# Performance work log

Measured on AMD Instinct MI355X. Metric: run time of the kernel, lower is better.

Reference implementation:

```python
import jax, jax.numpy as jnp
import numpy as np

L, B, T, TC, T1, D, DK, FF = 4, 4, 1024, 1024, 2048, 384, 256, 1536
TT = 0.1   # lamed blending coefficient (tt in (0,1] path)
EPS = 1e-5


def _ln(x, g, b):
    m = jnp.mean(x, axis=-1, keepdims=True)
    v = jnp.mean((x - m) ** 2, axis=-1, keepdims=True)
    return (x - m) * jax.lax.rsqrt(v + EPS) * g + b


def setup_inputs() -> dict:
    key = jax.random.key(0)
    ks = jax.random.split(key, 16)
    s = 0.02
    return {
        "tgt": jax.random.normal(ks[0], (B, T, D), jnp.float32),
        "memory": jax.random.normal(ks[1], (B, T1, DK), jnp.float32),
        "score_c": jax.random.normal(ks[2], (L, B, TC, T1), jnp.float32),
        "out_c": jax.random.normal(ks[3], (L, B, TC, D), jnp.float32),
        "Wq": jax.random.normal(ks[4], (L, D, D), jnp.float32) * s,
        "bq": jnp.zeros((L, D), jnp.float32),
        "Wk": jax.random.normal(ks[5], (L, D, DK), jnp.float32) * s,
        "bk": jnp.zeros((L, D), jnp.float32),
        "Wv": jax.random.normal(ks[6], (L, D, DK), jnp.float32) * s,
        "bv": jnp.zeros((L, D), jnp.float32),
        "Wkn": jax.random.normal(ks[7], (L, D, D), jnp.float32) * s,
        "bkn": jnp.zeros((L, D), jnp.float32),
        "Wun": jax.random.normal(ks[8], (L, D, D), jnp.float32) * s,
        "bun": jnp.zeros((L, D), jnp.float32),
        "W1": jax.random.normal(ks[9], (L, FF, D), jnp.float32) * s,
        "b1": jnp.zeros((L, FF), jnp.float32),
        "W2": jax.random.normal(ks[10], (L, D, FF), jnp.float32) * s,
        "b2": jnp.zeros((L, D), jnp.float32),
        "g1": jnp.ones((L, D), jnp.float32),
        "be1": jnp.zeros((L, D), jnp.float32),
        "g2": jnp.ones((L, D), jnp.float32),
        "be2": jnp.zeros((L, D), jnp.float32),
    }


def reference(tgt, memory, score_c, out_c, Wq, bq, Wk, bk, Wv, bv,
              Wkn, bkn, Wun, bun, W1, b1, W2, b2, g1, be1, g2, be2):
    scale = 1.0 / np.sqrt(D)
    x = tgt
    for l in range(L):  # fixed small layer count
        # cross-attention q/k/v (n_head = 1)
        q = jnp.einsum('btd,ed->bte', x, Wq[l]) + bq[l]            # [B,T,D]
        k = jnp.einsum('bsk,ek->bse', memory, Wk[l]) + bk[l]       # [B,T1,D]
        v = jnp.einsum('bsk,ek->bse', memory, Wv[l]) + bv[l]       # [B,T1,D]
        att = jnp.einsum('bte,bse->bts', q, k) * scale             # [B,T,T1]
        # blended score path (tt in (0,1])
        unk = jnp.einsum('btd,ed->bte', x, Wun[l]) + bun[l]        # [B,T,D]
        kno = jnp.einsum('bcd,ed->bce', out_c[l], Wkn[l]) + bkn[l] # [B,TC,D]
        score1 = jnp.einsum('bte,bce->btc', unk, kno) * scale      # [B,T,TC]
        mixed = jnp.einsum('btc,bcs->bts', score1, score_c[l])     # [B,T,T1]
        blended = TT * jax.nn.softmax(mixed, axis=-1) \
                  + (1.0 - TT) * jax.nn.softmax(att, axis=-1)
        z = jnp.einsum('bts,bse->bte', blended, v)                 # [B,T,D]
        x = _ln(x + z, g1[l], be1[l])
        h = jax.nn.relu(jnp.einsum('btd,fd->btf', x, W1[l]) + b1[l])
        y2 = jnp.einsum('btf,df->btd', h, W2[l]) + b2[l]
        x = _ln(x + y2, g2[l], be2[l])
    return x
```

## Files before the change

### kernel.cpp

```cpp
#include <hip/hip_runtime.h>
#include <math.h>

#define Lc 4
#define Bc 4
#define Tc 1024
#define TCc 1024
#define T1c 2048
#define Dc 384
#define DKc 256
#define FFc 1536
#define TTc 0.1f
#define EPSc 1e-5f

typedef unsigned short u16;
typedef __attribute__((ext_vector_type(8))) __bf16 bf16x8;
typedef __attribute__((ext_vector_type(4))) float f32x4;

__device__ inline u16 f2bf(float f) {
  union { float f; unsigned u; } x; x.f = f;
  unsigned r = x.u + 0x7fffu + ((x.u >> 16) & 1u);
  return (u16)(r >> 16);
}

struct CDesc { const float* src; u16* dst; long n4; };
struct CPack { CDesc d[16]; long tot4; int nd; };

__global__ void cvt_multi(CPack P) {
  long i = (long)blockIdx.x * 256 + threadIdx.x;
  const long st = (long)gridDim.x * 256;
  for (; i < P.tot4; i += st) {
    long r = i; int g = 0;
    while (g < P.nd - 1 && r >= P.d[g].n4) { r -= P.d[g].n4; ++g; }
    float4 v = ((const float4*)P.d[g].src)[r];
    ushort4 o;
    o.x = f2bf(v.x); o.y = f2bf(v.y); o.z = f2bf(v.z); o.w = f2bf(v.w);
    ((ushort4*)P.d[g].dst)[r] = o;
  }
}

__global__ void concat_bias(const float* __restrict__ a, const float* __restrict__ b,
                            float* __restrict__ o) {
  int l = blockIdx.x, t = threadIdx.x;
  o[l * 768 + t] = (t < Dc) ? a[l * Dc + t] : b[l * Dc + t - Dc];
}

__global__ __launch_bounds__(256) void transpose_cvt(const float* __restrict__ src,
                                                     u16* __restrict__ dst) {
  __shared__ float t[64 * 65];
  const int z = blockIdx.z;
  const float* s = src + (long)z * TCc * T1c;
  u16* d = dst + (long)z * T1c * TCc;
  const int s0 = blockIdx.x * 64, c0 = blockIdx.y * 64;
  const int tc = threadIdx.x >> 4;
  const int tx = (threadIdx.x & 15) * 4;
#pragma unroll
  for (int it = 0; it < 4; ++it) {
    const int c = tc + it * 16;
    float4 v = *(const float4*)(s + (long)(c0 + c) * T1c + s0 + tx);
    float* q = t + c * 65 + tx;
    q[0] = v.x; q[1] = v.y; q[2] = v.z; q[3] = v.w;
  }
  __syncthreads();
#pragma unroll
  for (int it = 0; it < 4; ++it) {
    const int srow = tc + it * 16;
    u16 o[4];
#pragma unroll
    for (int k2 = 0; k2 < 4; ++k2) o[k2] = f2bf(t[(tx + k2) * 65 + srow]);
    *(ushort4*)(d + (long)(s0 + srow) * TCc + c0 + tx) = *(ushort4*)o;
  }
}

template<int BIAS_MODE, int RELU, int OUT_MODE, int SWIZ>
__global__ __launch_bounds__(256) void gemm_bt(
    const u16* __restrict__ A, const u16* __restrict__ B,
    void* __restrict__ C, const float* __restrict__ bias,
    float alpha, int N, int K, int lda, int ldb,
    long sA, long sB, long sC, long sBias, int ksplit, long sSlab)
{
  __shared__ __attribute__((aligned(16))) u16 As[128 * 32];
  __shared__ __attribute__((aligned(16))) u16 Bs[128 * 32];
  const int bz = blockIdx.z;
  const int b = bz / ksplit;
  const int kc = bz - b * ksplit;
  const int Klen = K / ksplit;
  const int k0 = kc * Klen;
  const u16* Ab = A + (long)b * sA;
  const u16* Bb = B + (long)b * sB;
  long tm, tn;
  if (SWIZ) {
    const int id = blockIdx.y * 16 + blockIdx.x;
    tm = (long)(id >> 4) * 128;
    tn = (long)(2 * (id & 7) + ((id >> 3) & 1)) * 128;
  } else {
    tm = (long)blockIdx.y * 128; tn = (long)blockIdx.x * 128;
  }
  const int tid = threadIdx.x;
  const int lane = tid & 63, wv = tid >> 6;
  const int wm = (wv >> 1) * 64, wn = (wv & 1) * 64;
  const int q = lane >> 4, r = lane & 15;
  const int ldr = lane >> 2;
  const int ldc = (lane & 3) * 8;

  const u16* gA0 = Ab + (tm + wv * 32 + ldr) * (long)lda + k0 + ldc;
  const u16* gA1 = gA0 + 16 * (long)lda;
  const u16* gB0 = Bb + (tn + wv * 32 + ldr) * (long)ldb + k0 + ldc;
  const u16* gB1 = gB0 + 16 * (long)ldb;
  u16* dA0 = As + (wv * 32 + ldr) * 32 + ldc;
  u16* dA1 = dA0 + 16 * 32;
  u16* dB0 = Bs + (wv * 32 + ldr) * 32 + ldc;
  u16* dB1 = dB0 + 16 * 32;

  const f32x4 zero4 = {0.0f, 0.0f, 0.0f, 0.0f};
  f32x4 acc[4][4];
#pragma unroll
  for (int i = 0; i < 4; ++i)
#pragma unroll
    for (int j = 0; j < 4; ++j) acc[i][j] = zero4;

  uint4 ra0 = *(const uint4*)gA0;
  uint4 ra1 = *(const uint4*)gA1;
  uint4 rb0 = *(const uint4*)gB0;
  uint4 rb1 = *(const uint4*)gB1;

  const int iters = Klen >> 5;
  for (int it = 0; it < iters; ++it) {
    __builtin_amdgcn_s_barrier();
    *(uint4*)dA0 = ra0; *(uint4*)dA1 = ra1;
    *(uint4*)dB0 = rb0; *(uint4*)dB1 = rb1;
    __syncthreads();
    if (it + 1 < iters) {
      const long o = (long)(it + 1) * 32;
      ra0 = *(const uint4*)(gA0 + o);
      ra1 = *(const uint4*)(gA1 + o);
      rb0 = *(const uint4*)(gB0 + o);
      rb1 = *(const uint4*)(gB1 + o);
    }
    bf16x8 af[4], bfr[4];
#pragma unroll
    for (int i = 0; i < 4; ++i) {
      af[i]  = *(const bf16x8*)(As + (wm + i * 16 + r) * 32 + q * 8);
      bfr[i] = *(const bf16x8*)(Bs + (wn + i * 16 + r) * 32 + q * 8);
    }
#pragma unroll
    for (int i = 0; i < 4; ++i)
#pragma unroll
      for (int j = 0; j < 4; ++j)
        acc[i][j] = __builtin_amdgcn_mfma_f32_16x16x32_bf16(af[i], bfr[j], acc[i][j], 0, 0, 0);
  }

  const float* biasb = bias ? bias + (long)b * sBias : nullptr;
#pragma unroll
  for (int i = 0; i < 4; ++i)
#pragma unroll
    for (int j = 0; j < 4; ++j)
#pragma unroll
      for (int v = 0; v < 4; ++v) {
        long row = tm + wm + i * 16 + q * 4 + v;
        long col = tn + wn + j * 16 + r;
        float val = acc[i][j][v] * alpha;
        if (BIAS_MODE == 1 && kc == 0) val += biasb[col];
        if (BIAS_MODE == 2 && kc == 0) val += biasb[row];
        if (RELU) val = fmaxf(val, 0.0f);
        long idx = (long)kc * sSlab + (long)b * sC + row * (long)N + col;
        if (OUT_MODE == 0)      ((float*)C)[idx] = val;
        else if (OUT_MODE == 1) ((u16*)C)[idx] = f2bf(val);
        else                    ((_Float16*)C)[idx] = (_Float16)val;
      }
}

__global__ __launch_bounds__(256) void blend_softmax(
    const _Float16* __restrict__ att, const _Float16* __restrict__ mixed,
    u16* __restrict__ out)
{
  const long row = blockIdx.x;
  const int tid = threadIdx.x;
  const _Float16* ar = att + row * T1c;
  const _Float16* mr = mixed + row * T1c;
  float a[8], m[8];
#pragma unroll
  for (int i = 0; i < 8; ++i) {
    a[i] = (float)ar[tid + i * 256];
    m[i] = (float)mr[tid + i * 256];
  }
  float amax = a[0], mmax = m[0];
#pragma unroll
  for (int i = 1; i < 8; ++i) { amax = fmaxf(amax, a[i]); mmax = fmaxf(mmax, m[i]); }
#pragma unroll
  for (int off = 32; off > 0; off >>= 1) {
    amax = fmaxf(amax, __shfl_xor(amax, off));
    mmax = fmaxf(mmax, __shfl_xor(mmax, off));
  }
  __shared__ float red[8];
  const int lane = tid & 63, wv = tid >> 6;
  if (lane == 0) { red[wv] = amax; red[4 + wv] = mmax; }
  __syncthreads();
  amax = fmaxf(fmaxf(red[0], red[1]), fmaxf(red[2], red[3]));
  mmax = fmaxf(fmaxf(red[4], red[5]), fmaxf(red[6], red[7]));
  __syncthreads();
  float asum = 0.f, msum = 0.f;
#pragma unroll
  for (int i = 0; i < 8; ++i) {
    a[i] = __expf(a[i] - amax); asum += a[i];
    m[i] = __expf(m[i] - mmax); msum += m[i];
  }
#pragma unroll
  for (int off = 32; off > 0; off >>= 1) {
    asum += __shfl_xor(asum, off);
    msum += __shfl_xor(msum, off);
  }
  if (lane == 0) { red[wv] = asum; red[4 + wv] = msum; }
  __syncthreads();
  asum = red[0] + red[1] + red[2] + red[3];
  msum = red[4] + red[5] + red[6] + red[7];
  const float ca = (1.0f - TTc) / asum, cm = TTc / msum;
#pragma unroll
  for (int i = 0; i < 8; ++i)
    out[row * T1c + tid + i * 256] = f2bf(a[i] * ca + m[i] * cm);
}

__global__ __launch_bounds__(384) void add_ln4(
    const float* __restrict__ xin, const float* __restrict__ zs,
    const float* __restrict__ g, const float* __restrict__ be,
    float* __restrict__ xout, u16* __restrict__ xbf)
{
  const long row = blockIdx.x;
  const int d = threadIdx.x;
  const long SL = (long)Bc * Tc * Dc;
  const long o = row * Dc + d;
  float v = xin[o] + zs[o] + zs[SL + o] + zs[2 * SL + o] + zs[3 * SL + o];
  float s = v, s2 = v * v;
#pragma unroll
  for (int off = 32; off > 0; off >>= 1) {
    s  += __shfl_xor(s, off);
    s2 += __shfl_xor(s2, off);
  }
  __shared__ float red[12];
  const int lane = d & 63, wv = d >> 6;
  if (lane == 0) { red[wv] = s; red[6 + wv] = s2; }
  __syncthreads();
  float S = 0.f, S2 = 0.f;
#pragma unroll
  for (int w = 0; w < 6; ++w) { S += red[w]; S2 += red[6 + w]; }
  const float mean = S * (1.0f / Dc);
  const float var  = S2 * (1.0f / Dc) - mean * mean;
  const float rstd = rsqrtf(var + EPSc);
  const float y = (v - mean) * rstd * g[d] + be[d];
  xout[o] = y;
  xbf[o] = f2bf(y);
}

extern "C" void kernel_launch(void* const* d_in, const int* in_sizes, int n_in,
                              void* d_out, int out_size, void* d_ws, size_t ws_size,
                              hipStream_t stream)
{
  const float* tgt     = (const float*)d_in[0];
  const float* memory  = (const float*)d_in[1];
  const float* score_c = (const float*)d_in[2];
  const float* out_c   = (const float*)d_in[3];
  const float* Wq  = (const float*)d_in[4];  const float* bq  = (const float*)d_in[5];
  const float* Wk  = (const float*)d_in[6];  const float* bk  = (const float*)d_in[7];
  const float* Wv  = (const float*)d_in[8];  const float* bv  = (const float*)d_in[9];
  const float* Wkn = (const float*)d_in[10]; const float* bkn = (const float*)d_in[11];
  const float* Wun = (const float*)d_in[12]; const float* bun = (const float*)d_in[13];
  const float* W1  = (const float*)d_in[14]; const float* b1  = (const float*)d_in[15];
  const float* W2  = (const float*)d_in[16]; const float* b2  = (const float*)d_in[17];
  const float* g1  = (const float*)d_in[18]; const float* be1 = (const float*)d_in[19];
  const float* g2  = (const float*)d_in[20]; const float* be2 = (const float*)d_in[21];
  (void)in_sizes; (void)n_in; (void)out_size;

  char* p = (char*)d_ws;
  auto alloc = [&](size_t b) { char* r = p; p += (b + 255) & ~(size_t)255; return r; };

  u16* wk_bf   = (u16*)alloc((size_t)Lc * Dc * DKc * 2);
  u16* wv_bf   = (u16*)alloc((size_t)Lc * Dc * DKc * 2);
  u16* wkn_bf  = (u16*)alloc((size_t)Lc * Dc * Dc * 2);
  u16* w1_bf   = (u16*)alloc((size_t)Lc * FFc * Dc * 2);
  u16* w2_bf   = (u16*)alloc((size_t)Lc * Dc * FFc * 2);
  u16* wqu_bf  = (u16*)alloc((size_t)Lc * 2 * Dc * Dc * 2);
  float* bqu   = (float*)alloc((size_t)Lc * 2 * Dc * 4);
  u16* mem_bf  = (u16*)alloc((size_t)Bc * T1c * DKc * 2);
  u16* outc_bf = (u16*)alloc((size_t)Lc * Bc * TCc * Dc * 2);
  u16* x_bf    = (u16*)alloc((size_t)Bc * Tc * Dc * 2);
  float* xbuf  = (float*)alloc((size_t)Bc * Tc * Dc * 4);
  u16* qunk_bf = (u16*)alloc((size_t)Bc * Tc * 2 * Dc * 2);
  u16* k_all   = (u16*)alloc((size_t)Bc * T1c * Lc * Dc * 2);
  u16* vT_all  = (u16*)alloc((size_t)Bc * Lc * Dc * T1c * 2);
  u16* kno_all = (u16*)alloc((size_t)Lc * Bc * TCc * Dc * 2);
  u16* s1_bf   = (u16*)alloc((size_t)Bc * Tc * TCc * 2);
  u16* scT_all = (u16*)alloc((size_t)Lc * Bc * T1c * TCc * 2);
  _Float16* att   = (_Float16*)alloc((size_t)Bc * Tc * T1c * 2);
  _Float16* mixed = (_Float16*)alloc((size_t)Bc * Tc * T1c * 2);
  u16* blended = (u16*)alloc((size_t)Bc * Tc * T1c * 2);
  float* zslab = (float*)alloc((size_t)4 * Bc * Tc * Dc * 4);
  float* yslab = (float*)alloc((size_t)4 * Bc * Tc * Dc * 4);
  u16* h_bf    = (u16*)alloc((size_t)Bc * Tc * FFc * 2);

  if ((size_t)(p - (char*)d_ws) > ws_size) return;

  {
    CPack cp{}; int g = 0; long tot4 = 0;
    auto add = [&](const float* s, u16* d, long n) {
      cp.d[g].src = s; cp.d[g].dst = d; cp.d[g].n4 = n / 4; tot4 += n / 4; ++g;
    };
    add(Wk,  wk_bf,  (long)Lc * Dc * DKc);
    add(Wv,  wv_bf,  (long)Lc * Dc * DKc);
    add(Wkn, wkn_bf, (long)Lc * Dc * Dc);
    add(W1,  w1_bf,  (long)Lc * FFc * Dc);
    add(W2,  w2_bf,  (long)Lc * Dc * FFc);
    add(memory, mem_bf, (long)Bc * T1c * DKc);
    add(out_c, outc_bf, (long)Lc * Bc * TCc * Dc);
    add(tgt, x_bf, (long)Bc * Tc * Dc);
    for (int l = 0; l < Lc; ++l) {
      add(Wq + (long)l * Dc * Dc,  wqu_bf + (long)l * 2 * Dc * Dc, (long)Dc * Dc);
      add(Wun + (long)l * Dc * Dc, wqu_bf + (long)l * 2 * Dc * Dc + Dc * Dc, (long)Dc * Dc);
    }
    cp.nd = g; cp.tot4 = tot4;
    cvt_multi<<<4096, 256, 0, stream>>>(cp);
  }
  concat_bias<<<Lc, 2 * Dc, 0, stream>>>(bq, bun, bqu);

  transpose_cvt<<<dim3(T1c / 64, TCc / 64, Lc * Bc), 256, 0, stream>>>(score_c, scT_all);

  const float scale = 1.0f / sqrtf((float)Dc);
  const long SLAB = (long)Bc * Tc * Dc;

  gemm_bt<1,0,1,0><<<dim3(Lc*Dc/128, Bc*T1c/128, 1), 256, 0, stream>>>(
      mem_bf, wk_bf, k_all, bk, 1.0f, Lc*Dc, DKc, DKc, DKc, 0, 0, 0, 0, 1, 0);
  gemm_bt<2,0,1,0><<<dim3(T1c/128, Lc*Dc/128, Bc), 256, 0, stream>>>(
      wv_bf, mem_bf, vT_all, bv, 1.0f, T1c, DKc, DKc, DKc,
      0, (long)T1c*DKc, (long)Lc*Dc*T1c, 0, 1, 0);
  gemm_bt<1,0,1,0><<<dim3(Dc/128, Bc*TCc/128, Lc), 256, 0, stream>>>(
      outc_bf, wkn_bf, kno_all, bkn, 1.0f, Dc, Dc, Dc, Dc,
      (long)Bc*TCc*Dc, (long)Dc*Dc, (long)Bc*TCc*Dc, Dc, 1, 0);

  for (int l = 0; l < Lc; ++l) {
    gemm_bt<1,0,1,0><<<dim3(2*Dc/128, Bc*Tc/128, 1), 256, 0, stream>>>(
        x_bf, wqu_bf + (long)l*2*Dc*Dc, qunk_bf, bqu + l*2*Dc,
        1.0f, 2*Dc, Dc, Dc, Dc, 0, 0, 0, 0, 1, 0);
    gemm_bt<0,0,2,0><<<dim3(T1c/128, Tc/128, Bc), 256, 0, stream>>>(
        qunk_bf, k_all + l*Dc, att, nullptr, scale, T1c, Dc, 2*Dc, Lc*Dc,
        (long)Tc*2*Dc, (long)T1c*Lc*Dc, (long)Tc*T1c, 0, 1, 0);
    gemm_bt<0,0,1,0><<<dim3(TCc/128, Tc/128, Bc), 256, 0, stream>>>(
        qunk_bf + Dc, kno_all + (long)l*Bc*TCc*Dc, s1_bf, nullptr, scale,
        TCc, Dc, 2*Dc, Dc, (long)Tc*2*Dc, (long)TCc*Dc, (long)Tc*TCc, 0, 1, 0);
    gemm_bt<0,0,2,1><<<dim3(T1c/128, Tc/128, Bc), 256, 0, stream>>>(
        s1_bf, scT_all + (long)l*Bc*T1c*TCc, mixed, nullptr, 1.0f,
        T1c, TCc, TCc, TCc, (long)Tc*TCc, (long)T1c*TCc, (long)Tc*T1c, 0, 1, 0);
    blend_softmax<<<Bc*Tc, 256, 0, stream>>>(att, mixed, blended);
    gemm_bt<0,0,0,0><<<dim3(Dc/128, Tc/128, Bc*4), 256, 0, stream>>>(
        blended, vT_all + (long)l*Dc*T1c, zslab, nullptr, 1.0f,
        Dc, T1c, T1c, T1c, (long)Tc*T1c, (long)Lc*Dc*T1c, (long)Tc*Dc, 0, 4, SLAB);
    add_ln4<<<Bc*Tc, Dc, 0, stream>>>(
        (l == 0) ? tgt : xbuf, zslab, g1 + l*Dc, be1 + l*Dc, xbuf, x_bf);
    gemm_bt<1,1,1,0><<<dim3(FFc/128, Bc*Tc/128, 1), 256, 0, stream>>>(
        x_bf, w1_bf + (long)l*FFc*Dc, h_bf, b1 + l*FFc, 1.0f,
        FFc, Dc, Dc, Dc, 0, 0, 0, 0, 1, 0);
    gemm_bt<1,0,0,0><<<dim3(Dc/128, Bc*Tc/128, 4), 256, 0, stream>>>(
        h_bf, w2_bf + (long)l*Dc*FFc, yslab, b2 + l*Dc, 1.0f,
        Dc, FFc, FFc, FFc, 0, 0, 0, 0, 4, SLAB);
    add_ln4<<<Bc*Tc, Dc, 0, stream>>>(
        xbuf, yslab, g2 + l*Dc, be2 + l*Dc,
        (l == Lc - 1) ? (float*)d_out : xbuf, x_bf);
  }
}
```

Measured before the change: 1.024 ms.

## Load GEMM tiles via global_load_lds and vectorize blend softmax I/O

The GEMM main loop no longer stages tiles through registers with a software prefetch. It now issues direct global-to-LDS loads (global_load_lds, 16 bytes per lane) each iteration, with a barrier before and after the MFMA compute. Separately, the blend softmax kernel switches from strided scalar loads and stores to contiguous 8-wide vector loads and one 16-byte store per thread. The trade-off is that the register double-buffer prefetch is gone, so load latency is no longer hidden behind compute and an extra barrier is paid per iteration. The LDS layout written by the direct loads also has to match the layout the fragment reads expect.

```diff
diff --git a/kernel.cpp b/kernel.cpp
--- a/kernel.cpp
+++ b/kernel.cpp
@@ -14,12 +14,19 @@
 
 typedef unsigned short u16;
 typedef __attribute__((ext_vector_type(8))) __bf16 bf16x8;
+typedef __attribute__((ext_vector_type(8))) _Float16 f16x8;
 typedef __attribute__((ext_vector_type(4))) float f32x4;
 
 __device__ inline u16 f2bf(float f) {
   union { float f; unsigned u; } x; x.f = f;
   unsigned r = x.u + 0x7fffu + ((x.u >> 16) & 1u);
   return (u16)(r >> 16);
+}
+
+__device__ __forceinline__ void gld16(const u16* g, u16* l) {
+  __builtin_amdgcn_global_load_lds(
+      (__attribute__((address_space(1))) void*)g,
+      (__attribute__((address_space(3))) void*)l, 16, 0, 0);
 }
 
 struct CDesc { const float* src; u16* dst; long n4; };
@@ -106,10 +113,10 @@
   const u16* gA1 = gA0 + 16 * (long)lda;
   const u16* gB0 = Bb + (tn + wv * 32 + ldr) * (long)ldb + k0 + ldc;
   const u16* gB1 = gB0 + 16 * (long)ldb;
-  u16* dA0 = As + (wv * 32 + ldr) * 32 + ldc;
-  u16* dA1 = dA0 + 16 * 32;
-  u16* dB0 = Bs + (wv * 32 + ldr) * 32 + ldc;
-  u16* dB1 = dB0 + 16 * 32;
+  u16* dA0 = As + wv * 1024;
+  u16* dA1 = As + wv * 1024 + 512;
+  u16* dB0 = Bs + wv * 1024;
+  u16* dB1 = Bs + wv * 1024 + 512;
 
   const f32x4 zero4 = {0.0f, 0.0f, 0.0f, 0.0f};
   f32x4 acc[4][4];
@@ -118,24 +125,14 @@
 #pragma unroll
     for (int j = 0; j < 4; ++j) acc[i][j] = zero4;
 
-  uint4 ra0 = *(const uint4*)gA0;
-  uint4 ra1 = *(const uint4*)gA1;
-  uint4 rb0 = *(const uint4*)gB0;
-  uint4 rb1 = *(const uint4*)gB1;
-
   const int iters = Klen >> 5;
   for (int it = 0; it < iters; ++it) {
-    __builtin_amdgcn_s_barrier();
-    *(uint4*)dA0 = ra0; *(uint4*)dA1 = ra1;
-    *(uint4*)dB0 = rb0; *(uint4*)dB1 = rb1;
+    const long o = (long)it * 32;
+    gld16(gA0 + o, dA0);
+    gld16(gA1 + o, dA1);
+    gld16(gB0 + o, dB0);
+    gld16(gB1 + o, dB1);
     __syncthreads();
-    if (it + 1 < iters) {
-      const long o = (long)(it + 1) * 32;
-      ra0 = *(const uint4*)(gA0 + o);
-      ra1 = *(const uint4*)(gA1 + o);
-      rb0 = *(const uint4*)(gB0 + o);
-      rb1 = *(const uint4*)(gB1 + o);
-    }
     bf16x8 af[4], bfr[4];
 #pragma unroll
     for (int i = 0; i < 4; ++i) {
@@ -147,6 +144,7 @@
 #pragma unroll
       for (int j = 0; j < 4; ++j)
         acc[i][j] = __builtin_amdgcn_mfma_f32_16x16x32_bf16(af[i], bfr[j], acc[i][j], 0, 0, 0);
+    __syncthreads();
   }
 
   const float* biasb = bias ? bias + (long)b * sBias : nullptr;
@@ -175,14 +173,11 @@
 {
   const long row = blockIdx.x;
   const int tid = threadIdx.x;
-  const _Float16* ar = att + row * T1c;
-  const _Float16* mr = mixed + row * T1c;
+  f16x8 av = *(const f16x8*)(att + row * T1c + tid * 8);
+  f16x8 mv = *(const f16x8*)(mixed + row * T1c + tid * 8);
   float a[8], m[8];
 #pragma unroll
-  for (int i = 0; i < 8; ++i) {
-    a[i] = (float)ar[tid + i * 256];
-    m[i] = (float)mr[tid + i * 256];
-  }
+  for (int i = 0; i < 8; ++i) { a[i] = (float)av[i]; m[i] = (float)mv[i]; }
   float amax = a[0], mmax = m[0];
 #pragma unroll
   for (int i = 1; i < 8; ++i) { amax = fmaxf(amax, a[i]); mmax = fmaxf(mmax, m[i]); }
@@ -214,9 +209,10 @@
   asum = red[0] + red[1] + red[2] + red[3];
   msum = red[4] + red[5] + red[6] + red[7];
   const float ca = (1.0f - TTc) / asum, cm = TTc / msum;
-#pragma unroll
-  for (int i = 0; i < 8; ++i)
-    out[row * T1c + tid + i * 256] = f2bf(a[i] * ca + m[i] * cm);
+  u16 o[8];
+#pragma unroll
+  for (int i = 0; i < 8; ++i) o[i] = f2bf(a[i] * ca + m[i] * cm);
+  *(uint4*)(out + row * T1c + tid * 8) = *(uint4*)o;
 }
 
 __global__ __launch_bounds__(384) void add_ln4(
```

Result: slower. 1.115 ms (+8.8%).

## Reassociate mixed-score product to precompute score_c·kno outside the layer loop

Applied to the files above, without the earlier changes.

The blended-score path is reassociated as unk·(kno^T·score_c) instead of (unk·kno^T)·score_c. The layer-independent product M2 = score_c^T·kno (scaled) is computed once per layer and batch before the loop. Inside the loop a K=1024 GEMM and the score1 intermediate are replaced by a single K=384 GEMM. The gemm kernel gains a batch divisor for the A operand so weights can be shared across batches, and blend_softmax now uses vectorized 16-byte loads and stores. This adds a precompute GEMM and changes rounding, since M2 is stored in bf16.

```diff
diff --git a/kernel.cpp b/kernel.cpp
--- a/kernel.cpp
+++ b/kernel.cpp
@@ -14,6 +14,7 @@
 
 typedef unsigned short u16;
 typedef __attribute__((ext_vector_type(8))) __bf16 bf16x8;
+typedef __attribute__((ext_vector_type(8))) _Float16 f16x8;
 typedef __attribute__((ext_vector_type(4))) float f32x4;
 
 __device__ inline u16 f2bf(float f) {
@@ -76,16 +77,17 @@
     const u16* __restrict__ A, const u16* __restrict__ B,
     void* __restrict__ C, const float* __restrict__ bias,
     float alpha, int N, int K, int lda, int ldb,
-    long sA, long sB, long sC, long sBias, int ksplit, long sSlab)
+    long sA, long sB, long sC, long sBias, int ksplit, long sSlab, int bdivA)
 {
   __shared__ __attribute__((aligned(16))) u16 As[128 * 32];
   __shared__ __attribute__((aligned(16))) u16 Bs[128 * 32];
   const int bz = blockIdx.z;
   const int b = bz / ksplit;
   const int kc = bz - b * ksplit;
+  const int ba = b / bdivA;
   const int Klen = K / ksplit;
   const int k0 = kc * Klen;
-  const u16* Ab = A + (long)b * sA;
+  const u16* Ab = A + (long)ba * sA;
   const u16* Bb = B + (long)b * sB;
   long tm, tn;
   if (SWIZ) {
@@ -149,7 +151,7 @@
         acc[i][j] = __builtin_amdgcn_mfma_f32_16x16x32_bf16(af[i], bfr[j], acc[i][j], 0, 0, 0);
   }
 
-  const float* biasb = bias ? bias + (long)b * sBias : nullptr;
+  const float* biasb = bias ? bias + (long)ba * sBias : nullptr;
 #pragma unroll
   for (int i = 0; i < 4; ++i)
 #pragma unroll
@@ -175,14 +177,11 @@
 {
   const long row = blockIdx.x;
   const int tid = threadIdx.x;
-  const _Float16* ar = att + row * T1c;
-  const _Float16* mr = mixed + row * T1c;
+  f16x8 av = *(const f16x8*)(att + row * T1c + tid * 8);
+  f16x8 mv = *(const f16x8*)(mixed + row * T1c + tid * 8);
   float a[8], m[8];
 #pragma unroll
-  for (int i = 0; i < 8; ++i) {
-    a[i] = (float)ar[tid + i * 256];
-    m[i] = (float)mr[tid + i * 256];
-  }
+  for (int i = 0; i < 8; ++i) { a[i] = (float)av[i]; m[i] = (float)mv[i]; }
   float amax = a[0], mmax = m[0];
 #pragma unroll
   for (int i = 1; i < 8; ++i) { amax = fmaxf(amax, a[i]); mmax = fmaxf(mmax, m[i]); }
@@ -214,9 +213,10 @@
   asum = red[0] + red[1] + red[2] + red[3];
   msum = red[4] + red[5] + red[6] + red[7];
   const float ca = (1.0f - TTc) / asum, cm = TTc / msum;
-#pragma unroll
-  for (int i = 0; i < 8; ++i)
-    out[row * T1c + tid + i * 256] = f2bf(a[i] * ca + m[i] * cm);
+  u16 o[8];
+#pragma unroll
+  for (int i = 0; i < 8; ++i) o[i] = f2bf(a[i] * ca + m[i] * cm);
+  *(uint4*)(out + row * T1c + tid * 8) = *(uint4*)o;
 }
 
 __global__ __launch_bounds__(384) void add_ln4(
@@ -286,8 +286,8 @@
   u16* qunk_bf = (u16*)alloc((size_t)Bc * Tc * 2 * Dc * 2);
   u16* k_all   = (u16*)alloc((size_t)Bc * T1c * Lc * Dc * 2);
   u16* vT_all  = (u16*)alloc((size_t)Bc * Lc * Dc * T1c * 2);
-  u16* kno_all = (u16*)alloc((size_t)Lc * Bc * TCc * Dc * 2);
-  u16* s1_bf   = (u16*)alloc((size_t)Bc * Tc * TCc * 2);
+  u16* knoT_all = (u16*)alloc((size_t)Lc * Bc * Dc * TCc * 2);
+  u16* M2T_all = (u16*)alloc((size_t)Lc * Bc * T1c * Dc * 2);
   u16* scT_all = (u16*)alloc((size_t)Lc * Bc * T1c * TCc * 2);
   _Float16* att   = (_Float16*)alloc((size_t)Bc * Tc * T1c * 2);
   _Float16* mixed = (_Float16*)alloc((size_t)Bc * Tc * T1c * 2);
@@ -326,39 +326,39 @@
   const long SLAB = (long)Bc * Tc * Dc;
 
   gemm_bt<1,0,1,0><<<dim3(Lc*Dc/128, Bc*T1c/128, 1), 256, 0, stream>>>(
-      mem_bf, wk_bf, k_all, bk, 1.0f, Lc*Dc, DKc, DKc, DKc, 0, 0, 0, 0, 1, 0);
+      mem_bf, wk_bf, k_all, bk, 1.0f, Lc*Dc, DKc, DKc, DKc, 0, 0, 0, 0, 1, 0, 1);
   gemm_bt<2,0,1,0><<<dim3(T1c/128, Lc*Dc/128, Bc), 256, 0, stream>>>(
       wv_bf, mem_bf, vT_all, bv, 1.0f, T1c, DKc, DKc, DKc,
-      0, (long)T1c*DKc, (long)Lc*Dc*T1c, 0, 1, 0);
-  gemm_bt<1,0,1,0><<<dim3(Dc/128, Bc*TCc/128, Lc), 256, 0, stream>>>(
-      outc_bf, wkn_bf, kno_all, bkn, 1.0f, Dc, Dc, Dc, Dc,
-      (long)Bc*TCc*Dc, (long)Dc*Dc, (long)Bc*TCc*Dc, Dc, 1, 0);
+      0, (long)T1c*DKc, (long)Lc*Dc*T1c, 0, 1, 0, 1);
+  gemm_bt<2,0,1,0><<<dim3(TCc/128, Dc/128, Lc*Bc), 256, 0, stream>>>(
+      wkn_bf, outc_bf, knoT_all, bkn, 1.0f, TCc, Dc, Dc, Dc,
+      (long)Dc*Dc, (long)TCc*Dc, (long)Dc*TCc, Dc, 1, 0, Bc);
+  gemm_bt<0,0,1,0><<<dim3(Dc/128, T1c/128, Lc*Bc), 256, 0, stream>>>(
+      scT_all, knoT_all, M2T_all, nullptr, scale, Dc, TCc, TCc, TCc,
+      (long)T1c*TCc, (long)Dc*TCc, (long)T1c*Dc, 0, 1, 0, 1);
 
   for (int l = 0; l < Lc; ++l) {
     gemm_bt<1,0,1,0><<<dim3(2*Dc/128, Bc*Tc/128, 1), 256, 0, stream>>>(
         x_bf, wqu_bf + (long)l*2*Dc*Dc, qunk_bf, bqu + l*2*Dc,
-        1.0f, 2*Dc, Dc, Dc, Dc, 0, 0, 0, 0, 1, 0);
+        1.0f, 2*Dc, Dc, Dc, Dc, 0, 0, 0, 0, 1, 0, 1);
     gemm_bt<0,0,2,0><<<dim3(T1c/128, Tc/128, Bc), 256, 0, stream>>>(
         qunk_bf, k_all + l*Dc, att, nullptr, scale, T1c, Dc, 2*Dc, Lc*Dc,
-        (long)Tc*2*Dc, (long)T1c*Lc*Dc, (long)Tc*T1c, 0, 1, 0);
-    gemm_bt<0,0,1,0><<<dim3(TCc/128, Tc/128, Bc), 256, 0, stream>>>(
-        qunk_bf + Dc, kno_all + (long)l*Bc*TCc*Dc, s1_bf, nullptr, scale,
-        TCc, Dc, 2*Dc, Dc, (long)Tc*2*Dc, (long)TCc*Dc, (long)Tc*TCc, 0, 1, 0);
+        (long)Tc*2*Dc, (long)T1c*Lc*Dc, (long)Tc*T1c, 0, 1, 0, 1);
     gemm_bt<0,0,2,1><<<dim3(T1c/128, Tc/128, Bc), 256, 0, stream>>>(
-        s1_bf, scT_all + (long)l*Bc*T1c*TCc, mixed, nullptr, 1.0f,
-        T1c, TCc, TCc, TCc, (long)Tc*TCc, (long)T1c*TCc, (long)Tc*T1c, 0, 1, 0);
+        qunk_bf + Dc, M2T_all + (long)l*Bc*T1c*Dc, mixed, nullptr, 1.0f,
+        T1c, Dc, 2*Dc, Dc, (long)Tc*2*Dc, (long)T1c*Dc, (long)Tc*T1c, 0, 1, 0, 1);
     blend_softmax<<<Bc*Tc, 256, 0, stream>>>(att, mixed, blended);
     gemm_bt<0,0,0,0><<<dim3(Dc/128, Tc/128, Bc*4), 256, 0, stream>>>(
         blended, vT_all + (long)l*Dc*T1c, zslab, nullptr, 1.0f,
-        Dc, T1c, T1c, T1c, (long)Tc*T1c, (long)Lc*Dc*T1c, (long)Tc*Dc, 0, 4, SLAB);
+        Dc, T1c, T1c, T1c, (long)Tc*T1c, (long)Lc*Dc*T1c, (long)Tc*Dc, 0, 4, SLAB, 1);
     add_ln4<<<Bc*Tc, Dc, 0, stream>>>(
         (l == 0) ? tgt : xbuf, zslab, g1 + l*Dc, be1 + l*Dc, xbuf, x_bf);
     gemm_bt<1,1,1,0><<<dim3(FFc/128, Bc*Tc/128, 1), 256, 0, stream>>>(
         x_bf, w1_bf + (long)l*FFc*Dc, h_bf, b1 + l*FFc, 1.0f,
-        FFc, Dc, Dc, Dc, 0, 0, 0, 0, 1, 0);
+        FFc, Dc, Dc, Dc, 0, 0, 0, 0, 1, 0, 1);
     gemm_bt<1,0,0,0><<<dim3(Dc/128, Bc*Tc/128, 4), 256, 0, stream>>>(
         h_bf, w2_bf + (long)l*Dc*FFc, yslab, b2 + l*Dc, 1.0f,
-        Dc, FFc, FFc, FFc, 0, 0, 0, 0, 4, SLAB);
+        Dc, FFc, FFc, FFc, 0, 0, 0, 0, 4, SLAB, 1);
     add_ln4<<<Bc*Tc, Dc, 0, stream>>>(
         xbuf, yslab, g2 + l*Dc, be2 + l*Dc,
         (l == Lc - 1) ? (float*)d_out : xbuf, x_bf);
```

After: 975.1 us. 4.8% less time.
